# Performance work log

Hardware: AMD Instinct MI355X
Metric: run time of the kernel (lower is better)

The kernel has to match this reference:

```python
import math
import jax, jax.numpy as jnp
import numpy as np

HID, HEADS, HEAD_DIM, MLP = 768, 12, 64, 3072
ROT_AXIS = HEAD_DIM // 4  # 16 rotary dims per spatial axis, 48 total
MAX_FREQ = 256.0
EPS_GN, EPS_LN = 1e-6, 1e-5


def setup_inputs() -> dict:
    key = jax.random.key(0)
    ks = jax.random.split(key, 5)
    B, H, W, D = 2, 12, 12, 12
    s = 0.02
    return {
        "x": jax.random.normal(ks[0], (B, HID, H, W, D), jnp.float32),
        "norm1_w": jnp.ones((HID,), jnp.float32),
        "w_fused": jax.random.normal(ks[1], (MLP + 3 * HID, HID), jnp.float32) * s,
        "b_fused": jnp.zeros((MLP + 3 * HID,), jnp.float32),
        "q_gamma": jnp.ones((HEAD_DIM,), jnp.float32),
        "q_beta": jnp.zeros((HEAD_DIM,), jnp.float32),
        "k_gamma": jnp.ones((HEAD_DIM,), jnp.float32),
        "k_beta": jnp.zeros((HEAD_DIM,), jnp.float32),
        "w_attn": jax.random.normal(ks[2], (HID, HID), jnp.float32) * s,
        "w_ff": jax.random.normal(ks[3], (HID, MLP // 2), jnp.float32) * s,
        "b_ff": jnp.zeros((HID,), jnp.float32),
    }


def _layernorm(t, gamma, beta):
    mu = jnp.mean(t, axis=-1, keepdims=True)
    var = jnp.mean((t - mu) ** 2, axis=-1, keepdims=True)
    return (t - mu) / jnp.sqrt(var + EPS_LN) * gamma + beta


def _rotate_half(t):
    # interleaved pairs: (x1, x2) -> (-x2, x1)
    t2 = t.reshape(t.shape[:-1] + (t.shape[-1] // 2, 2))
    return jnp.stack((-t2[..., 1], t2[..., 0]), axis=-1).reshape(t.shape)


def _axial_freqs(H, W, D):
    base = jnp.linspace(1.0, MAX_FREQ / 2, ROT_AXIS // 2) * math.pi  # (8,)
    def ax(n):
        pos = jnp.linspace(-1.0, 1.0, n)
        f = pos[:, None] * base[None, :]          # (n, 8)
        return jnp.repeat(f, 2, axis=-1)          # (n, 16)
    fH = jnp.broadcast_to(ax(H)[:, None, None, :], (H, W, D, ROT_AXIS))
    fW = jnp.broadcast_to(ax(W)[None, :, None, :], (H, W, D, ROT_AXIS))
    fD = jnp.broadcast_to(ax(D)[None, None, :, :], (H, W, D, ROT_AXIS))
    return jnp.concatenate((fH, fW, fD), axis=-1)  # (H, W, D, 48)


def _apply_rope(t, cosf, sinf, rot_dim):
    t_mid, t_right = t[..., :rot_dim], t[..., rot_dim:]
    t_mid = t_mid * cosf + _rotate_half(t_mid) * sinf
    return jnp.concatenate((t_mid, t_right), axis=-1)


def reference(x, norm1_w, w_fused, b_fused, q_gamma, q_beta, k_gamma, k_beta,
              w_attn, w_ff, b_ff):
    B, C, H, W, D = x.shape
    residual = x
    # RMSGroupNorm: norm axes are the spatial dims only (per-channel RMS)
    rms = jnp.sqrt(jnp.mean(x ** 2, axis=(2, 3, 4), keepdims=True) + EPS_GN)
    xn = x / rms * norm1_w[None, :, None, None, None]
    xn = jnp.transpose(xn, (0, 2, 3, 4, 1))  # b h w d c
    fused = jnp.einsum('bhwdc,oc->bhwdo', xn, w_fused) + b_fused
    ff = fused[..., :MLP]
    q = fused[..., MLP:MLP + HID]
    k = fused[..., MLP + HID:MLP + 2 * HID]
    v = fused[..., MLP + 2 * HID:]
    def to_heads(t):  # b h w d (he c) -> b he h w d c
        return jnp.transpose(t.reshape(B, H, W, D, HEADS, HEAD_DIM), (0, 4, 1, 2, 3, 5))
    q, k, v = to_heads(q), to_heads(k), to_heads(v)
    q = _layernorm(q, q_gamma, q_beta)
    k = _layernorm(k, k_gamma, k_beta)
    freqs = _axial_freqs(H, W, D)                 # (H, W, D, 48)
    cosf, sinf = jnp.cos(freqs), jnp.sin(freqs)
    rot_dim = freqs.shape[-1]
    q = _apply_rope(q, cosf, sinf, rot_dim)
    k = _apply_rope(k, cosf, sinf, rot_dim)
    S = H * W * D
    q = q.reshape(B, HEADS, S, HEAD_DIM)
    k = k.reshape(B, HEADS, S, HEAD_DIM)
    v = v.reshape(B, HEADS, S, HEAD_DIM)
    scale = 1.0 / math.sqrt(HEAD_DIM)
    attn = jax.nn.softmax(jnp.einsum('bhsc,bhtc->bhst', q, k) * scale, axis=-1)
    att = jnp.einsum('bhst,bhtc->bhsc', attn, v)
    att = jnp.transpose(att, (0, 2, 1, 3)).reshape(B, H, W, D, HID)
    attn_out = jnp.einsum('bhwdc,oc->bhwdo', att, w_attn)
    ff_x, gate = jnp.split(ff, 2, axis=-1)
    ff_act = jax.nn.silu(gate) * ff_x
    ff_out = jnp.einsum('bhwdc,oc->bhwdo', ff_act, w_ff) + b_ff
    out = attn_out + ff_out
    out = jnp.transpose(out, (0, 4, 1, 2, 3)) + residual
    return out
```

## Files before the change

kernel.cpp:

```cpp
#include <hip/hip_runtime.h>

using bf16 = __bf16;
typedef __attribute__((ext_vector_type(8))) __bf16 bf16x8;
typedef __attribute__((ext_vector_type(4))) float f32x4;

#define HID    768
#define S_TOT  1728
#define MLP_   3072
#define NFUSED 5376
#define HEADS  12
#define HDIM   64
#define ROT    48
#define KCAT   2304

__device__ __forceinline__ void gload16(const void* g, void* l) {
  __builtin_amdgcn_global_load_lds((__attribute__((address_space(1))) void*)g,
                                   (__attribute__((address_space(3))) void*)l,
                                   16, 0, 0);
}

__device__ __forceinline__ float fexp2(float x) {
  float r; asm("v_exp_f32 %0, %1" : "=v"(r) : "v"(x)); return r;
}

__device__ __forceinline__ float wsum64(float v) {
  #pragma unroll
  for (int d = 32; d; d >>= 1) v += __shfl_xor(v, d);
  return v;
}

__global__ __launch_bounds__(256) void k_conv(const float* __restrict__ wf,
    const float* __restrict__ wa, const float* __restrict__ wff,
    bf16* __restrict__ owf, bf16* __restrict__ wcat) {
  int i = blockIdx.x * 256 + threadIdx.x;
  const int nf = NFUSED * HID, na = HID * HID, nff = HID * (MLP_ / 2);
  if (i < nf)  owf[i] = (bf16)wf[i];
  if (i < na)  wcat[(i / HID) * KCAT + (i % HID)] = (bf16)wa[i];
  if (i < nff) wcat[(i / (MLP_ / 2)) * KCAT + HID + (i % (MLP_ / 2))] = (bf16)wff[i];
}

__global__ __launch_bounds__(256) void k_rms(const float* __restrict__ x,
    const float* __restrict__ w, float* __restrict__ scale) {
  int bc = blockIdx.x;
  const float* xp = x + (size_t)bc * S_TOT;
  float s = 0.f;
  for (int i = threadIdx.x; i < S_TOT; i += 256) { float v = xp[i]; s += v * v; }
  s = wsum64(s);
  __shared__ float red[4];
  int lane = threadIdx.x & 63, wv = threadIdx.x >> 6;
  if (lane == 0) red[wv] = s;
  __syncthreads();
  if (threadIdx.x == 0) {
    float t = red[0] + red[1] + red[2] + red[3];
    scale[bc] = w[bc % HID] * rsqrtf(t * (1.f / S_TOT) + 1e-6f);
  }
}

__global__ __launch_bounds__(256) void k_xpose(const float* __restrict__ x,
    const float* __restrict__ scale, bf16* __restrict__ xn) {
  __shared__ float t[32][33];
  int b = blockIdx.z, st = blockIdx.x * 32, ct = blockIdx.y * 32;
  int tx = threadIdx.x & 31, ty = threadIdx.x >> 5;
  #pragma unroll
  for (int i = 0; i < 4; ++i) {
    int c = ct + ty + i * 8;
    t[ty + i * 8][tx] = x[((size_t)b * HID + c) * S_TOT + st + tx] * scale[b * HID + c];
  }
  __syncthreads();
  #pragma unroll
  for (int i = 0; i < 4; ++i) {
    int s = st + ty + i * 8;
    xn[((size_t)b * S_TOT + s) * HID + ct + tx] = (bf16)t[tx][ty + i * 8];
  }
}

__global__ __launch_bounds__(256) void k_rope(float* __restrict__ ct, float* __restrict__ st) {
  int i = blockIdx.x * 256 + threadIdx.x;
  if (i >= S_TOT * ROT) return;
  int s = i / ROT, j = i % ROT;
  int axis = j >> 4, pr = (j & 15) >> 1;
  float base = 3.14159265358979323846f * (1.f + pr * (127.f / 7.f));
  int coord = axis == 0 ? (s / 144) : axis == 1 ? ((s / 12) % 12) : (s % 12);
  float pos = -1.f + coord * (2.f / 11.f);
  float f = pos * base;
  ct[i] = cosf(f); st[i] = sinf(f);
}

template <int BN, int MODE, int NMAJOR, int MINB, int BUFS>
__global__ __launch_bounds__(256, MINB) void k_gemm(const bf16* __restrict__ A,
    const bf16* __restrict__ Bw, const float* __restrict__ bias,
    void* __restrict__ OutV, const float* __restrict__ X, int M, int N, int K) {
  extern __shared__ __align__(16) char smem[];
  bf16* aL = (bf16*)smem;
  bf16* bL = (bf16*)(smem + BUFS * 8192);
  constexpr int NT = BN / 32;
  constexpr int LPS = 2 + BN / 64;
  const int nT = K / 32;
  int nwg = gridDim.x;
  int cq = nwg >> 3, crr = nwg & 7;
  int xcd = blockIdx.x & 7, pos = blockIdx.x >> 3;
  int idx = (xcd < crr ? xcd * (cq + 1) : crr * (cq + 1) + (xcd - crr) * cq) + pos;
  int ntn = N / BN, nmt = M / 128;
  int m0, n0;
  if (NMAJOR) { n0 = (idx / nmt) * BN; m0 = (idx % nmt) * 128; }
  else        { m0 = (idx / ntn) * 128; n0 = (idx % ntn) * BN; }
  int lane = threadIdx.x & 63, wv = threadIdx.x >> 6;
  int wm = (wv >> 1) * 64, wn = (wv & 1) * (BN / 2);
  int arow = lane >> 2;
  int acs = ((lane & 3) ^ ((lane >> 3) & 3)) * 8;
  int r16 = lane & 15, g8 = (lane >> 4) * 8;
  int swz = ((r16 >> 1) & 3) << 3;
  const bf16* Ag = A + (size_t)m0 * K;
  const bf16* Bg = Bw + (size_t)n0 * K;
  auto stage = [&](int p, int t) {
    int kk = t * 32;
    #pragma unroll
    for (int i = 0; i < 2; ++i) {
      int rb = wv * 32 + i * 16;
      gload16(Ag + (size_t)(rb + arow) * K + kk + acs, aL + p * 4096 + rb * 32);
    }
    #pragma unroll
    for (int i = 0; i < BN / 64; ++i) {
      int rb = wv * (BN / 4) + i * 16;
      gload16(Bg + (size_t)(rb + arow) * K + kk + acs, bL + p * (BN * 32) + rb * 32);
    }
  };
  f32x4 acc[4][NT] = {};
  int p = 0;
  if constexpr (BUFS == 3) { stage(0, 0); stage(1, 1); }
  else                     { stage(0, 0); }
  for (int t = 0; t < nT; ++t) {
    if constexpr (BUFS == 2) {
      if (t + 1 < nT) {
        stage(p ^ 1, t + 1);
        if constexpr (LPS == 5) asm volatile("s_waitcnt vmcnt(5)\ns_barrier" ::: "memory");
        else if constexpr (LPS == 4) asm volatile("s_waitcnt vmcnt(4)\ns_barrier" ::: "memory");
        else                     asm volatile("s_waitcnt vmcnt(3)\ns_barrier" ::: "memory");
      } else {
        asm volatile("s_waitcnt vmcnt(0)\ns_barrier" ::: "memory");
      }
    } else {
      if (t + 1 < nT) {
        if constexpr (LPS == 6)      asm volatile("s_waitcnt vmcnt(6)\ns_barrier" ::: "memory");
        else if constexpr (LPS == 4) asm volatile("s_waitcnt vmcnt(4)\ns_barrier" ::: "memory");
        else                         asm volatile("s_waitcnt vmcnt(3)\ns_barrier" ::: "memory");
      } else {
        asm volatile("s_waitcnt vmcnt(0)\ns_barrier" ::: "memory");
      }
      if (t + 2 < nT) { int pn = p + 2; if (pn >= 3) pn -= 3; stage(pn, t + 2); }
    }
    bf16x8 af[4], bfr[NT];
    #pragma unroll
    for (int mi = 0; mi < 4; ++mi)
      af[mi] = *(const bf16x8*)(aL + p * 4096 + (wm + mi * 16 + r16) * 32 + (g8 ^ swz));
    #pragma unroll
    for (int ni = 0; ni < NT; ++ni)
      bfr[ni] = *(const bf16x8*)(bL + p * (BN * 32) + (wn + ni * 16 + r16) * 32 + (g8 ^ swz));
    __builtin_amdgcn_s_setprio(1);
    #pragma unroll
    for (int mi = 0; mi < 4; ++mi)
      #pragma unroll
      for (int ni = 0; ni < NT; ++ni)
        acc[mi][ni] = __builtin_amdgcn_mfma_f32_16x16x32_bf16(af[mi], bfr[ni], acc[mi][ni], 0, 0, 0);
    __builtin_amdgcn_s_setprio(0);
    if constexpr (BUFS == 2) {
      asm volatile("s_barrier" ::: "memory");
      p ^= 1;
    } else {
      if (++p == 3) p = 0;
    }
  }
  int cr = (lane >> 4) * 4;
  if constexpr (MODE == 0) {
    #pragma unroll
    for (int mi = 0; mi < 4; ++mi)
      #pragma unroll
      for (int ni = 0; ni < NT; ++ni) {
        int col = n0 + wn + ni * 16 + r16;
        float bv = bias[col];
        #pragma unroll
        for (int j = 0; j < 4; ++j) {
          int row = m0 + wm + mi * 16 + cr + j;
          ((bf16*)OutV)[(size_t)row * N + col] = (bf16)(acc[mi][ni][j] + bv);
        }
      }
  } else {
    float* tb = (float*)smem;
    __syncthreads();
    #pragma unroll
    for (int mi = 0; mi < 4; ++mi)
      #pragma unroll
      for (int ni = 0; ni < NT; ++ni) {
        int c = wn + ni * 16 + r16;
        float bv = bias[n0 + c];
        #pragma unroll
        for (int j = 0; j < 4; ++j)
          tb[c * 129 + wm + mi * 16 + cr + j] = acc[mi][ni][j] + bv;
      }
    __syncthreads();
    float* Out = (float*)OutV;
    for (int ci = 0; ci < BN / 4; ++ci) {
      int c = wv * (BN / 4) + ci;
      #pragma unroll
      for (int si = 0; si < 2; ++si) {
        int r = si * 64 + lane;
        int m = m0 + r;
        int bb = (m >= S_TOT) ? 1 : 0;
        size_t oidx = ((size_t)bb * HID + n0 + c) * S_TOT + (m - bb * S_TOT);
        Out[oidx] = tb[c * 129 + r] + X[oidx];
      }
    }
  }
}

__global__ __launch_bounds__(256) void k_silu(const bf16* __restrict__ fused, bf16* __restrict__ acat) {
  int idx = blockIdx.x * 256 + threadIdx.x;
  if (idx >= 3456 * 192) return;
  int r = idx / 192, jg = idx % 192;
  bf16x8 xv = *(const bf16x8*)(fused + (size_t)r * NFUSED + jg * 8);
  bf16x8 gv = *(const bf16x8*)(fused + (size_t)r * NFUSED + (MLP_ / 2) + jg * 8);
  bf16x8 o;
  #pragma unroll
  for (int j = 0; j < 8; ++j) {
    float g  = (float)gv[j];
    float xf = (float)xv[j];
    o[j] = (bf16)(g / (1.f + __expf(-g)) * xf);
  }
  *(bf16x8*)(acat + (size_t)r * KCAT + HID + jg * 8) = o;
}

__global__ __launch_bounds__(256) void k_qkv(const bf16* __restrict__ fused,
    const float* __restrict__ ct, const float* __restrict__ st,
    const float* __restrict__ qg, const float* __restrict__ qb,
    const float* __restrict__ kg, const float* __restrict__ kb,
    bf16* __restrict__ qr, bf16* __restrict__ kr, bf16* __restrict__ vt) {
  int bs = blockIdx.x;
  int b = bs / S_TOT, s = bs % S_TOT;
  int lane = threadIdx.x & 63, wv = threadIdx.x >> 6;
  int d = lane;
  float c = 0.f, sn = 0.f;
  if (d < ROT) { c = ct[s * ROT + d]; sn = st[s * ROT + d]; }
  for (int it = 0; it < 9; ++it) {
    int rr = wv * 9 + it;
    int t = rr / HEADS, h = rr % HEADS;
    float v = (float)fused[(size_t)bs * NFUSED + MLP_ + t * HID + h * HDIM + d];
    if (t < 2) {
      float s1 = v, s2 = v * v;
      #pragma unroll
      for (int dd = 32; dd; dd >>= 1) { s1 += __shfl_xor(s1, dd); s2 += __shfl_xor(s2, dd); }
      float mu = s1 * (1.f / 64);
      float var = s2 * (1.f / 64) - mu * mu;
      float vn = (v - mu) * rsqrtf(var + 1e-5f);
      vn = (t == 0) ? (vn * qg[d] + qb[d]) : (vn * kg[d] + kb[d]);
      float o = vn;
      if (d < ROT) {
        float p = __shfl_xor(vn, 1);
        float rot = (d & 1) ? p : -p;
        o = vn * c + rot * sn;
      }
      if (t == 0) o *= 0.18033688f;
      bf16* dst = (t == 0) ? qr : kr;
      dst[((size_t)(b * HEADS + h) * S_TOT + s) * HDIM + d] = (bf16)o;
    } else {
      vt[((size_t)(b * HEADS + h) * HDIM + d) * S_TOT + s] = (bf16)v;
    }
  }
}

__global__ __launch_bounds__(256, 4) void k_attn(const bf16* __restrict__ qr,
    const bf16* __restrict__ kr, const bf16* __restrict__ vt, bf16* __restrict__ acat) {
  __shared__ __align__(16) bf16 kld[2][4096];
  __shared__ __align__(16) bf16 vld[2][4096];
  __shared__ __align__(16) bf16 pld[4][1024];
  int rid = (blockIdx.x & 7) * 81 + (blockIdx.x >> 3);
  int bh = rid / 27, qt = rid % 27;
  int lane = threadIdx.x & 63, wv = threadIdx.x >> 6;
  int r16 = lane & 15, g8 = (lane >> 4) * 8;
  int sw = (r16 & 7) << 3;
  int lsw = (lane & 56) | ((lane ^ (lane >> 3)) & 7);
  const bf16* qbase = qr + ((size_t)bh * S_TOT + qt * 64 + wv * 16) * HDIM;
  bf16x8 qf[2];
  qf[0] = *(const bf16x8*)(qbase + r16 * HDIM + g8);
  qf[1] = *(const bf16x8*)(qbase + r16 * HDIM + 32 + g8);
  asm volatile("s_waitcnt vmcnt(0)" ::: "memory");
  const bf16* kg0 = kr + (size_t)bh * S_TOT * HDIM;
  const bf16* vg0 = vt + (size_t)bh * HDIM * S_TOT;
  auto stage = [&](int buf, int kt) {
    #pragma unroll
    for (int i = 0; i < 2; ++i) {
      int q = wv * 2 + i;
      gload16(kg0 + (size_t)kt * 4096 + q * 512 + lsw * 8, &kld[buf][q * 512]);
      gload16(vg0 + (size_t)(q * 8 + (lane >> 3)) * S_TOT + kt * 64 + (lsw & 7) * 8,
              &vld[buf][q * 512]);
    }
  };
  float m_run[4] = {-1e30f, -1e30f, -1e30f, -1e30f};
  float l_part[4] = {0.f, 0.f, 0.f, 0.f};
  f32x4 acc_o[4] = {};
  stage(0, 0);
  int buf = 0;
  for (int kt = 0; kt < 27; ++kt) {
    if (kt < 26) {
      stage(buf ^ 1, kt + 1);
      asm volatile("s_waitcnt vmcnt(4)\n\ts_barrier" ::: "memory");
    } else {
      asm volatile("s_waitcnt vmcnt(0)\n\ts_barrier" ::: "memory");
    }
    f32x4 sa[4];
    __builtin_amdgcn_s_setprio(1);
    #pragma unroll
    for (int nt = 0; nt < 4; ++nt) {
      sa[nt] = f32x4{0.f, 0.f, 0.f, 0.f};
      #pragma unroll
      for (int kc = 0; kc < 2; ++kc) {
        bf16x8 kf = *(const bf16x8*)(&kld[buf][(nt * 16 + r16) * 64 + ((kc * 32 + g8) ^ sw)]);
        sa[nt] = __builtin_amdgcn_mfma_f32_16x16x32_bf16(qf[kc], kf, sa[nt], 0, 0, 0);
      }
    }
    __builtin_amdgcn_s_setprio(0);
    float lmax[4];
    #pragma unroll
    for (int j = 0; j < 4; ++j)
      lmax[j] = fmaxf(fmaxf(sa[0][j], sa[1][j]), fmaxf(sa[2][j], sa[3][j]));
    bool need = (lmax[0] > m_run[0] + 8.f) || (lmax[1] > m_run[1] + 8.f) ||
                (lmax[2] > m_run[2] + 8.f) || (lmax[3] > m_run[3] + 8.f);
    if (__any(need)) {
      float fac[4];
      #pragma unroll
      for (int j = 0; j < 4; ++j) {
        float tm = lmax[j];
        #pragma unroll
        for (int dd = 1; dd < 16; dd <<= 1) tm = fmaxf(tm, __shfl_xor(tm, dd));
        float mnew = fmaxf(m_run[j], tm);
        fac[j] = fexp2(m_run[j] - mnew);
        m_run[j] = mnew;
        l_part[j] *= fac[j];
      }
      #pragma unroll
      for (int nt = 0; nt < 4; ++nt)
        #pragma unroll
        for (int j = 0; j < 4; ++j) acc_o[nt][j] *= fac[j];
    }
    #pragma unroll
    for (int j = 0; j < 4; ++j) {
      float m = m_run[j];
      #pragma unroll
      for (int nt = 0; nt < 4; ++nt) {
        float pv = fexp2(sa[nt][j] - m);
        sa[nt][j] = pv;
        l_part[j] += pv;
      }
    }
    #pragma unroll
    for (int nt = 0; nt < 4; ++nt)
      #pragma unroll
      for (int j = 0; j < 4; ++j) {
        int rr = (lane >> 4) * 4 + j;
        pld[wv][rr * 64 + ((nt * 16 + r16) ^ ((rr & 7) << 3))] = (bf16)sa[nt][j];
      }
    __builtin_amdgcn_s_setprio(1);
    #pragma unroll
    for (int nt = 0; nt < 4; ++nt)
      #pragma unroll
      for (int kc = 0; kc < 2; ++kc) {
        bf16x8 pf = *(const bf16x8*)(&pld[wv][r16 * 64 + ((kc * 32 + g8) ^ sw)]);
        bf16x8 vf = *(const bf16x8*)(&vld[buf][(nt * 16 + r16) * 64 + ((kc * 32 + g8) ^ sw)]);
        acc_o[nt] = __builtin_amdgcn_mfma_f32_16x16x32_bf16(pf, vf, acc_o[nt], 0, 0, 0);
      }
    __builtin_amdgcn_s_setprio(0);
    asm volatile("s_barrier" ::: "memory");
    buf ^= 1;
  }
  int b = bh / HEADS, h = bh % HEADS;
  #pragma unroll
  for (int j = 0; j < 4; ++j) {
    float l = l_part[j];
    #pragma unroll
    for (int dd = 1; dd < 16; dd <<= 1) l += __shfl_xor(l, dd);
    float inv = 1.f / l;
    int s = qt * 64 + wv * 16 + (lane >> 4) * 4 + j;
    #pragma unroll
    for (int nt = 0; nt < 4; ++nt)
      acat[((size_t)b * S_TOT + s) * KCAT + h * HDIM + nt * 16 + r16] = (bf16)(acc_o[nt][j] * inv);
  }
}

extern "C" void kernel_launch(void* const* d_in, const int* in_sizes, int n_in,
                              void* d_out, int out_size, void* d_ws, size_t ws_size,
                              hipStream_t stream) {
  const float* x   = (const float*)d_in[0];
  const float* n1w = (const float*)d_in[1];
  const float* wf  = (const float*)d_in[2];
  const float* bfu = (const float*)d_in[3];
  const float* qg  = (const float*)d_in[4];
  const float* qb  = (const float*)d_in[5];
  const float* kg  = (const float*)d_in[6];
  const float* kb  = (const float*)d_in[7];
  const float* wa  = (const float*)d_in[8];
  const float* wff = (const float*)d_in[9];
  const float* bff = (const float*)d_in[10];
  float* out = (float*)d_out;

  char* ws = (char*)d_ws;
  size_t off = 0;
  auto alloc = [&](size_t bytes) {
    void* p = ws + off;
    off = (off + bytes + 255) & ~(size_t)255;
    return p;
  };
  const int M = 2 * S_TOT;
  bf16*  wf_b   = (bf16*)alloc((size_t)NFUSED * HID * 2);
  bf16*  wcat   = (bf16*)alloc((size_t)HID * KCAT * 2);
  float* scale  = (float*)alloc(2 * HID * 4);
  bf16*  xn     = (bf16*)alloc((size_t)M * HID * 2);
  float* ctab   = (float*)alloc((size_t)S_TOT * ROT * 4);
  float* stab   = (float*)alloc((size_t)S_TOT * ROT * 4);
  bf16*  fused  = (bf16*)alloc((size_t)M * NFUSED * 2);
  bf16*  qrb    = (bf16*)alloc((size_t)24 * S_TOT * HDIM * 2);
  bf16*  krb    = (bf16*)alloc((size_t)24 * S_TOT * HDIM * 2);
  bf16*  vtb    = (bf16*)alloc((size_t)24 * HDIM * S_TOT * 2);
  bf16*  acat   = (bf16*)alloc((size_t)M * KCAT * 2);
  if (off > ws_size) return;

  const int LDS_QKV = 2 * 8192 + 2 * 192 * 32 * 2;
  const int LDS_MRG = 3 * 8192 + 3 * 64 * 32 * 2;
  hipFuncSetAttribute((const void*)k_gemm<192, 0, 1, 3, 2>, hipFuncAttributeMaxDynamicSharedMemorySize, LDS_QKV);
  hipFuncSetAttribute((const void*)k_gemm<64, 2, 0, 4, 3>, hipFuncAttributeMaxDynamicSharedMemorySize, LDS_MRG);

  k_conv<<<(NFUSED * HID + 255) / 256, 256, 0, stream>>>(wf, wa, wff, wf_b, wcat);
  k_rms<<<2 * HID, 256, 0, stream>>>(x, n1w, scale);
  k_xpose<<<dim3(S_TOT / 32, HID / 32, 2), 256, 0, stream>>>(x, scale, xn);
  k_rope<<<(S_TOT * ROT + 255) / 256, 256, 0, stream>>>(ctab, stab);
  k_gemm<192, 0, 1, 3, 2><<<(M / 128) * (NFUSED / 192), 256, LDS_QKV, stream>>>(
      xn, wf_b, bfu, fused, nullptr, M, NFUSED, HID);
  k_silu<<<(M * (MLP_ / 2) / 8 + 255) / 256, 256, 0, stream>>>(fused, acat);
  k_qkv<<<M, 256, 0, stream>>>(fused, ctab, stab, qg, qb, kg, kb, qrb, krb, vtb);
  k_attn<<<648, 256, 0, stream>>>(qrb, krb, vtb, acat);
  k_gemm<64, 2, 0, 4, 3><<<(M / 128) * (HID / 64), 256, LDS_MRG, stream>>>(
      acat, wcat, bff, out, x, M, HID, KCAT);
}
```

Measured before the change: 167.3 us.

## Use single-wave attention blocks loading K/V directly from global memory

```diff
diff --git a/kernel.cpp b/kernel.cpp
--- a/kernel.cpp
+++ b/kernel.cpp
@@ -267,55 +267,41 @@
   }
 }
 
-__global__ __launch_bounds__(256, 4) void k_attn(const bf16* __restrict__ qr,
+__global__ __launch_bounds__(64, 3) void k_attn(const bf16* __restrict__ qr,
     const bf16* __restrict__ kr, const bf16* __restrict__ vt, bf16* __restrict__ acat) {
-  __shared__ __align__(16) bf16 kld[2][4096];
-  __shared__ __align__(16) bf16 vld[2][4096];
-  __shared__ __align__(16) bf16 pld[4][1024];
-  int rid = (blockIdx.x & 7) * 81 + (blockIdx.x >> 3);
-  int bh = rid / 27, qt = rid % 27;
-  int lane = threadIdx.x & 63, wv = threadIdx.x >> 6;
+  __shared__ __align__(16) bf16 pld[1024];
+  int rid = (blockIdx.x & 7) * 324 + (blockIdx.x >> 3);
+  int bh = rid / 108, q16 = rid % 108;
+  int lane = threadIdx.x & 63;
   int r16 = lane & 15, g8 = (lane >> 4) * 8;
   int sw = (r16 & 7) << 3;
-  int lsw = (lane & 56) | ((lane ^ (lane >> 3)) & 7);
-  const bf16* qbase = qr + ((size_t)bh * S_TOT + qt * 64 + wv * 16) * HDIM;
+  const bf16* qbase = qr + ((size_t)bh * S_TOT + q16 * 16) * HDIM;
   bf16x8 qf[2];
   qf[0] = *(const bf16x8*)(qbase + r16 * HDIM + g8);
   qf[1] = *(const bf16x8*)(qbase + r16 * HDIM + 32 + g8);
-  asm volatile("s_waitcnt vmcnt(0)" ::: "memory");
-  const bf16* kg0 = kr + (size_t)bh * S_TOT * HDIM;
-  const bf16* vg0 = vt + (size_t)bh * HDIM * S_TOT;
-  auto stage = [&](int buf, int kt) {
-    #pragma unroll
-    for (int i = 0; i < 2; ++i) {
-      int q = wv * 2 + i;
-      gload16(kg0 + (size_t)kt * 4096 + q * 512 + lsw * 8, &kld[buf][q * 512]);
-      gload16(vg0 + (size_t)(q * 8 + (lane >> 3)) * S_TOT + kt * 64 + (lsw & 7) * 8,
-              &vld[buf][q * 512]);
-    }
-  };
+  const bf16* kb = kr + (size_t)bh * S_TOT * HDIM;
+  const bf16* vb = vt + (size_t)bh * HDIM * S_TOT;
   float m_run[4] = {-1e30f, -1e30f, -1e30f, -1e30f};
   float l_part[4] = {0.f, 0.f, 0.f, 0.f};
   f32x4 acc_o[4] = {};
-  stage(0, 0);
-  int buf = 0;
   for (int kt = 0; kt < 27; ++kt) {
-    if (kt < 26) {
-      stage(buf ^ 1, kt + 1);
-      asm volatile("s_waitcnt vmcnt(4)\n\ts_barrier" ::: "memory");
-    } else {
-      asm volatile("s_waitcnt vmcnt(0)\n\ts_barrier" ::: "memory");
+    const bf16* kp = kb + kt * 64 * HDIM;
+    const bf16* vp = vb + kt * 64;
+    bf16x8 kf[4][2], vf[4][2];
+    #pragma unroll
+    for (int nt = 0; nt < 4; ++nt) {
+      kf[nt][0] = *(const bf16x8*)(kp + (nt * 16 + r16) * HDIM + g8);
+      kf[nt][1] = *(const bf16x8*)(kp + (nt * 16 + r16) * HDIM + 32 + g8);
+      vf[nt][0] = *(const bf16x8*)(vp + (size_t)(nt * 16 + r16) * S_TOT + g8);
+      vf[nt][1] = *(const bf16x8*)(vp + (size_t)(nt * 16 + r16) * S_TOT + 32 + g8);
     }
     f32x4 sa[4];
     __builtin_amdgcn_s_setprio(1);
     #pragma unroll
     for (int nt = 0; nt < 4; ++nt) {
-      sa[nt] = f32x4{0.f, 0.f, 0.f, 0.f};
-      #pragma unroll
-      for (int kc = 0; kc < 2; ++kc) {
-        bf16x8 kf = *(const bf16x8*)(&kld[buf][(nt * 16 + r16) * 64 + ((kc * 32 + g8) ^ sw)]);
-        sa[nt] = __builtin_amdgcn_mfma_f32_16x16x32_bf16(qf[kc], kf, sa[nt], 0, 0, 0);
-      }
+      sa[nt] = __builtin_amdgcn_mfma_f32_16x16x32_bf16(qf[0], kf[nt][0],
+                   f32x4{0.f, 0.f, 0.f, 0.f}, 0, 0, 0);
+      sa[nt] = __builtin_amdgcn_mfma_f32_16x16x32_bf16(qf[1], kf[nt][1], sa[nt], 0, 0, 0);
     }
     __builtin_amdgcn_s_setprio(0);
     float lmax[4];
@@ -356,20 +342,18 @@
       #pragma unroll
       for (int j = 0; j < 4; ++j) {
         int rr = (lane >> 4) * 4 + j;
-        pld[wv][rr * 64 + ((nt * 16 + r16) ^ ((rr & 7) << 3))] = (bf16)sa[nt][j];
-      }
+        pld[rr * 64 + ((nt * 16 + r16) ^ ((rr & 7) << 3))] = (bf16)sa[nt][j];
+      }
+    bf16x8 pf[2];
+    pf[0] = *(const bf16x8*)(&pld[r16 * 64 + ((g8) ^ sw)]);
+    pf[1] = *(const bf16x8*)(&pld[r16 * 64 + ((32 + g8) ^ sw)]);
     __builtin_amdgcn_s_setprio(1);
     #pragma unroll
-    for (int nt = 0; nt < 4; ++nt)
-      #pragma unroll
-      for (int kc = 0; kc < 2; ++kc) {
-        bf16x8 pf = *(const bf16x8*)(&pld[wv][r16 * 64 + ((kc * 32 + g8) ^ sw)]);
-        bf16x8 vf = *(const bf16x8*)(&vld[buf][(nt * 16 + r16) * 64 + ((kc * 32 + g8) ^ sw)]);
-        acc_o[nt] = __builtin_amdgcn_mfma_f32_16x16x32_bf16(pf, vf, acc_o[nt], 0, 0, 0);
-      }
+    for (int nt = 0; nt < 4; ++nt) {
+      acc_o[nt] = __builtin_amdgcn_mfma_f32_16x16x32_bf16(pf[0], vf[nt][0], acc_o[nt], 0, 0, 0);
+      acc_o[nt] = __builtin_amdgcn_mfma_f32_16x16x32_bf16(pf[1], vf[nt][1], acc_o[nt], 0, 0, 0);
+    }
     __builtin_amdgcn_s_setprio(0);
-    asm volatile("s_barrier" ::: "memory");
-    buf ^= 1;
   }
   int b = bh / HEADS, h = bh % HEADS;
   #pragma unroll
@@ -378,7 +362,7 @@
     #pragma unroll
     for (int dd = 1; dd < 16; dd <<= 1) l += __shfl_xor(l, dd);
     float inv = 1.f / l;
-    int s = qt * 64 + wv * 16 + (lane >> 4) * 4 + j;
+    int s = q16 * 16 + (lane >> 4) * 4 + j;
     #pragma unroll
     for (int nt = 0; nt < 4; ++nt)
       acat[((size_t)b * S_TOT + s) * KCAT + h * HDIM + nt * 16 + r16] = (bf16)(acc_o[nt][j] * inv);
@@ -435,7 +419,7 @@
       xn, wf_b, bfu, fused, nullptr, M, NFUSED, HID);
   k_silu<<<(M * (MLP_ / 2) / 8 + 255) / 256, 256, 0, stream>>>(fused, acat);
   k_qkv<<<M, 256, 0, stream>>>(fused, ctab, stab, qg, qb, kg, kb, qrb, krb, vtb);
-  k_attn<<<648, 256, 0, stream>>>(qrb, krb, vtb, acat);
+  k_attn<<<2592, 64, 0, stream>>>(qrb, krb, vtb, acat);
   k_gemm<64, 2, 0, 4, 3><<<(M / 128) * (HID / 64), 256, LDS_MRG, stream>>>(
       acat, wcat, bff, out, x, M, HID, KCAT);
 }
```

New measurement: 259.4 us. 1.55x slower.
